# Kernel tuning notes

Hardware: AMD Instinct MI355X
Metric: run time of the kernel (lower is better)

Reference implementation:

```python
import jax, jax.numpy as jnp
import numpy as np

T, B, OBS, H, A = 256, 128, 512, 1024, 18


def setup_inputs() -> dict:
    key = jax.random.key(0)
    ks = jax.random.split(key, 9)
    s = 0.02
    return {
        "state": jax.random.normal(ks[0], (T, B, OBS), dtype=jnp.float32),
        "mask": jax.random.randint(ks[1], (T, B), 0, 2, dtype=jnp.int32),
        "W_enc": jax.random.normal(ks[2], (H, OBS), dtype=jnp.float32) * s,
        "b_enc": jnp.zeros((H,), dtype=jnp.float32),
        "W_ih": jax.random.normal(ks[3], (4 * H, H), dtype=jnp.float32) * s,
        "W_hh": jax.random.normal(ks[4], (4 * H, H), dtype=jnp.float32) * s,
        "b_ih": jnp.zeros((4 * H,), dtype=jnp.float32),
        "b_hh": jnp.zeros((4 * H,), dtype=jnp.float32),
        "W_dec": jax.random.normal(ks[5], (A, H), dtype=jnp.float32) * s,
        "b_dec": jnp.zeros((A,), dtype=jnp.float32),
    }


def reference(state, mask, W_enc, b_enc, W_ih, W_hh, b_ih, b_hh, W_dec, b_dec):
    maskf = mask.astype(state.dtype)  # (T, B)
    hidden = W_hh.shape[1]
    # encode all timesteps in one GEMM: (T,B,OBS) @ (OBS,H)
    encoded = jax.nn.relu(jnp.einsum('tbo,ho->tbh', state, W_enc) + b_enc)
    # precompute input contribution to all gates (T,B,4H)
    x_gates = jnp.einsum('tbh,gh->tbg', encoded, W_ih) + b_ih + b_hh
    h0 = jnp.zeros((state.shape[1], hidden), dtype=state.dtype)
    c0 = jnp.zeros_like(h0)

    def step(carry, inp):
        h, c = carry
        xg, m = inp  # xg: (B,4H), m: (B,)
        gates = xg + h @ W_hh.T
        i, f, g, o = jnp.split(gates, 4, axis=-1)  # PyTorch LSTMCell gate order
        i = jax.nn.sigmoid(i)
        f = jax.nn.sigmoid(f)
        g = jnp.tanh(g)
        o = jax.nn.sigmoid(o)
        c_new = (f * c + i * g) * m[:, None]
        h_new = (o * jnp.tanh(f * c + i * g)) * m[:, None]
        return (h_new, c_new), h_new

    (h, c), latent = jax.lax.scan(step, (h0, c0), (x_gates, maskf))
    # decode all timesteps in one GEMM, then apply mask
    values = jnp.einsum('tbh,ah->tba', latent, W_dec) + b_dec
    values = values * maskf[:, :, None]
    return values, h, c
```

## Files before the change

### kernel.cpp

```cpp
#include <hip/hip_runtime.h>

#define T_STEPS 256
#define BATCH   128
#define OBSD    512
#define HID     1024
#define GH      4096
#define ACTD    18
#define TBROWS  (T_STEPS*BATCH)
#define SNWG    512
#define JG      16

typedef __bf16 bf16x8_t __attribute__((ext_vector_type(8)));
typedef float  f32x4_t  __attribute__((ext_vector_type(4)));

__device__ __forceinline__ ushort f2bf(float f) {
  unsigned u = __builtin_bit_cast(unsigned, f);
  u += 0x7fffu + ((u >> 16) & 1u);
  return (ushort)(u >> 16);
}
__device__ __forceinline__ float bf2f(ushort s) {
  return __builtin_bit_cast(float, ((unsigned)s) << 16);
}
__device__ __forceinline__ f32x4_t mfma16(bf16x8_t a, bf16x8_t b, f32x4_t c) {
  return __builtin_amdgcn_mfma_f32_16x16x32_bf16(a, b, c, 0, 0, 0);
}
__device__ __forceinline__ void gl_lds16(const void* g, void* l) {
  __builtin_amdgcn_global_load_lds(
      (__attribute__((address_space(1))) void*)(g),
      (__attribute__((address_space(3))) void*)(l), 16, 0, 0);
}
__device__ __forceinline__ float sigm(float x) { return 1.f / (1.f + __expf(-x)); }
__device__ __forceinline__ float tanhf_fast(float x) {
  float e = __expf(2.f * x);
  return (e - 1.f) / (e + 1.f);
}
#define WAITVM(N) __builtin_amdgcn_s_waitcnt(0x0F70 | ((N) & 15))
__device__ __forceinline__ void wait_vm0() { __builtin_amdgcn_s_waitcnt(0x0F70); }

__global__ void cast_bf16_kernel(const float* __restrict__ in, ushort* __restrict__ out, int n4) {
  int i = blockIdx.x * blockDim.x + threadIdx.x;
  int stride = gridDim.x * blockDim.x;
  for (; i < n4; i += stride) {
    float4 v = reinterpret_cast<const float4*>(in)[i];
    ushort4 o;
    o.x = f2bf(v.x); o.y = f2bf(v.y); o.z = f2bf(v.z); o.w = f2bf(v.w);
    reinterpret_cast<ushort4*>(out)[i] = o;
  }
}

__global__ void cast_permute_wih_kernel(const float* __restrict__ in, ushort* __restrict__ out) {
  int idx = blockIdx.x * 256 + threadIdx.x;
  int rowd = idx >> 7;
  int c8 = (idx & 127) << 3;
  int g = rowd & 3, hid = rowd >> 2;
  const float* src = in + ((size_t)g * HID + hid) * HID + c8;
  ushort* dst = out + (size_t)rowd * HID + c8;
#pragma unroll
  for (int i = 0; i < 8; ++i) dst[i] = f2bf(src[i]);
}

__global__ void bias_perm_kernel(const float* __restrict__ bih, const float* __restrict__ bhh,
                                 float* __restrict__ out) {
  int i = blockIdx.x * 256 + threadIdx.x;
  int g = i & 3, hid = i >> 2;
  out[i] = bih[g * HID + hid] + bhh[g * HID + hid];
}

__global__ __launch_bounds__(256) void gemm_bt_kernel(
    const ushort* __restrict__ A, const ushort* __restrict__ Bt,
    const float* __restrict__ bias1,
    ushort* __restrict__ C, int M, int N, int K, int relu,
    const int* __restrict__ omask, float* __restrict__ ovals)
{
  __shared__ ushort la[128 * 64];
  __shared__ ushort lb[128 * 64];

  const int tid  = threadIdx.x;
  const int lane = tid & 63;
  const int w    = tid >> 6;
  const int wm   = w >> 1, wn = w & 1;
  const int nwg = gridDim.x;
  const int q8  = nwg >> 3;
  const int bid = (blockIdx.x & 7) * q8 + (blockIdx.x >> 3);
  const int ntiles = N >> 7;
  const int bm = bid / ntiles, bn = bid % ntiles;
  const size_t m0 = (size_t)bm << 7, n0 = (size_t)bn << 7;

  const int lrow = lane & 15;
  const int lk   = (lane >> 4) << 3;
  const int wavebase = (tid & ~63);

  f32x4_t acc[4][4];
  const f32x4_t zero = {0.f, 0.f, 0.f, 0.f};
#pragma unroll
  for (int i = 0; i < 4; ++i)
#pragma unroll
    for (int j = 0; j < 4; ++j) acc[i][j] = zero;

  for (int k0 = 0; k0 < K; k0 += 64) {
#pragma unroll
    for (int p = 0; p < 4; ++p) {
      int c = p * 256 + tid;
      int r = c >> 3;
      int q = (c & 7) << 3;
      gl_lds16(A + (m0 + r) * (size_t)K + k0 + q, la + (size_t)(p * 256 + wavebase) * 8);
      gl_lds16(Bt + (n0 + r) * (size_t)K + k0 + q, lb + (size_t)(p * 256 + wavebase) * 8);
    }
    __syncthreads();
#pragma unroll
    for (int kk = 0; kk < 64; kk += 32) {
      bf16x8_t af[4], bfr[4];
#pragma unroll
      for (int i = 0; i < 4; ++i)
        af[i] = *(const bf16x8_t*)(la + (wm * 64 + i * 16 + lrow) * 64 + kk + lk);
#pragma unroll
      for (int j = 0; j < 4; ++j)
        bfr[j] = *(const bf16x8_t*)(lb + (wn * 64 + j * 16 + lrow) * 64 + kk + lk);
#pragma unroll
      for (int i = 0; i < 4; ++i)
#pragma unroll
        for (int j = 0; j < 4; ++j)
          acc[i][j] = mfma16(af[i], bfr[j], acc[i][j]);
    }
    __syncthreads();
  }

  const int crow0 = (lane >> 4) * 4;
  if (ovals) {
#pragma unroll
    for (int j = 0; j < 4; ++j) {
      int col = wn * 64 + j * 16 + lrow;
      if (col < ACTD) {
        float bv = bias1[col];
#pragma unroll
        for (int i = 0; i < 4; ++i) {
#pragma unroll
          for (int r = 0; r < 4; ++r) {
            size_t row = m0 + wm * 64 + i * 16 + crow0 + r;
            float mv = (float)omask[row];
            ovals[row * ACTD + col] = (acc[i][j][r] + bv) * mv;
          }
        }
      }
    }
    return;
  }
#pragma unroll
  for (int j = 0; j < 4; ++j) {
    int col = (int)n0 + wn * 64 + j * 16 + lrow;
    float bv = bias1 ? bias1[col] : 0.f;
#pragma unroll
    for (int i = 0; i < 4; ++i) {
#pragma unroll
      for (int r = 0; r < 4; ++r) {
        size_t row = m0 + wm * 64 + i * 16 + crow0 + r;
        float v = acc[i][j][r] + bv;
        if (relu) v = fmaxf(v, 0.f);
        C[row * (size_t)N + col] = f2bf(v);
      }
    }
  }
}

__global__ __launch_bounds__(512, 2) void gemm256_kernel(
    const ushort* __restrict__ A, const ushort* __restrict__ Bt,
    const float* __restrict__ bias,
    ushort* __restrict__ C, int M, int N, int K, int relu)
{
  __shared__ __align__(16) ushort lds[2][2][16384];

  const int tid  = threadIdx.x;
  const int lane = tid & 63;
  const int wid  = tid >> 6;
  const int wm   = wid >> 2, wn = wid & 3;
  const int nwg  = gridDim.x;
  const int q8   = nwg >> 3;
  const int bid  = (blockIdx.x & 7) * q8 + (blockIdx.x >> 3);
  const int ntiles = N >> 8;
  const int bm = bid / ntiles, bn = bid % ntiles;
  const size_t m0 = (size_t)bm << 8, n0 = (size_t)bn << 8;

  const int lrow = lane & 15;
  const int lkg  = lane >> 4;

  int srow[4], sgsr[4];
#pragma unroll
  for (int q = 0; q < 4; ++q) {
    int s = (q * 8 + wid) * 64 + lane;
    srow[q] = s >> 3;
    sgsr[q] = (s & 7) ^ ((s >> 3) & 7);
  }

#define STAGE256(BUF, KT) do {                                                \
    const size_t kb_ = (size_t)(KT) * 64;                                     \
    _Pragma("unroll")                                                         \
    for (int q = 0; q < 4; ++q) {                                             \
      gl_lds16(A  + (m0 + srow[q]) * (size_t)K + kb_ + sgsr[q] * 8,           \
               &lds[BUF][0][(q * 8 + wid) * 512]);                            \
      gl_lds16(Bt + (n0 + srow[q]) * (size_t)K + kb_ + sgsr[q] * 8,           \
               &lds[BUF][1][(q * 8 + wid) * 512]);                            \
    }                                                                         \
  } while (0)

  f32x4_t acc[8][4];
  const f32x4_t zero = {0.f, 0.f, 0.f, 0.f};
#pragma unroll
  for (int f = 0; f < 8; ++f)
#pragma unroll
    for (int n = 0; n < 4; ++n) acc[f][n] = zero;

  const int nkt = K >> 6;
  STAGE256(0, 0);
  STAGE256(1, 1);

  for (int kt = 0; kt < nkt; ++kt) {
    const int buf = kt & 1;
    if (kt + 1 < nkt) WAITVM(8); else WAITVM(0);
    __builtin_amdgcn_s_barrier();
    __builtin_amdgcn_sched_barrier(0);
#pragma unroll
    for (int p = 0; p < 4; ++p) {
      const int kk = p >> 1, mg = p & 1;
      bf16x8_t av[4], bv[4];
#pragma unroll
      for (int f = 0; f < 4; ++f) {
        int ar = wm * 128 + (mg * 4 + f) * 16 + lrow;
        int ags = (kk * 4 + lkg) ^ (ar & 7);
        av[f] = *(const bf16x8_t*)&lds[buf][0][ar * 64 + ags * 8];
      }
#pragma unroll
      for (int n = 0; n < 4; ++n) {
        int br = wn * 64 + n * 16 + lrow;
        int bgs = (kk * 4 + lkg) ^ (br & 7);
        bv[n] = *(const bf16x8_t*)&lds[buf][1][br * 64 + bgs * 8];
      }
      __builtin_amdgcn_s_setprio(1);
#pragma unroll
      for (int f = 0; f < 4; ++f)
#pragma unroll
        for (int n = 0; n < 4; ++n)
          acc[mg * 4 + f][n] = mfma16(av[f], bv[n], acc[mg * 4 + f][n]);
      __builtin_amdgcn_s_setprio(0);
    }
    __builtin_amdgcn_s_barrier();
    if (kt + 2 < nkt) STAGE256(buf, kt + 2);
  }
#undef STAGE256

  const int crow0 = lkg * 4;
#pragma unroll
  for (int n = 0; n < 4; ++n) {
    int col = (int)n0 + wn * 64 + n * 16 + lrow;
    float bvv = bias ? bias[col] : 0.f;
#pragma unroll
    for (int f = 0; f < 8; ++f) {
#pragma unroll
      for (int r = 0; r < 4; ++r) {
        size_t row = m0 + (size_t)wm * 128 + f * 16 + crow0 + r;
        float v = acc[f][n][r] + bvv;
        if (relu) v = fmaxf(v, 0.f);
        C[row * (size_t)N + col] = f2bf(v);
      }
    }
  }
}

__global__ __launch_bounds__(256, 2) void lstm_scan_kernel(
    const ushort* __restrict__ xg,
    const ushort* __restrict__ whh,
    const int* __restrict__ mask,
    const ushort* __restrict__ hinit,
    ushort* __restrict__ hseq,
    float* __restrict__ cbuf,
    float* __restrict__ outh, float* __restrict__ outc,
    unsigned* __restrict__ flags,
    int t0, int nsteps)
{
  __shared__ __align__(16) ushort pool[16 * 1024];
  __shared__ __align__(16) ushort hexch[16 * 16];

  const int tid  = threadIdx.x;
  const int lane = tid & 63;
  const int w    = tid >> 6;
  const int wg   = blockIdx.x;
  const int eg   = wg >> 6;
  const int jg   = wg & 63;
  const int j0   = jg * JG;
  const int b0   = eg * 16;

  const int lrow = lane & 15;
  const int lkg  = lane >> 4;

  bf16x8_t af[8][4];
#pragma unroll 1
  for (int p = 0; p < 4; ++p) {
    for (int c = tid; c < 16 * 128; c += 256) {
      int rl = c >> 7, gn = c & 127;
      int rr = p * 16 + rl;
      int jj = rr >> 2, g = rr & 3;
      const ushort* src = whh + ((size_t)g * HID + j0 + jj) * HID + gn * 8;
      int gnd = (gn & ~7) | ((gn & 7) ^ (rl & 7));
      *reinterpret_cast<uint4*>(&pool[rl * 1024 + gnd * 8]) =
          *reinterpret_cast<const uint4*>(src);
    }
    __syncthreads();
    if (w == p) {
#pragma unroll
      for (int kc = 0; kc < 8; ++kc)
#pragma unroll
        for (int ks = 0; ks < 4; ++ks) {
          int gA = kc * 16 + ks * 4 + lkg;
          int gAs = (gA & ~7) | ((gA & 7) ^ (lrow & 7));
          af[kc][ks] = *(const bf16x8_t*)(pool + (size_t)lrow * 1024 + gAs * 8);
        }
    }
    __syncthreads();
  }

  const int jjc = w * 4 + lkg;
  const int bl0 = lrow;

  float creg;
  if (t0 == 0) creg = 0.f;
  else creg = cbuf[(size_t)(b0 + bl0) * HID + j0 + jjc];

  const int sb = w * 4 + (lane >> 4);
  const int sq = lane & 15;
  const int gg = (sq & 8) | ((sq & 7) ^ (sb & 7));

  unsigned* myflag = flags + (size_t)(eg * 64 + jg) * 16;
  const unsigned* fpoll = flags + (size_t)(eg * 64 + lane) * 16;

  ushort4 xv;
  float mv;
  {
    xv = *(const ushort4*)(xg + (size_t)(b0 + bl0) * GH + (j0 + jjc) * 4);
    mv = (float)mask[b0 + bl0];
  }
  __builtin_amdgcn_sched_barrier(0);

#define CHUNK(KC) do {                                                         \
    WAITVM(7 - (KC));                                                          \
    __builtin_amdgcn_s_barrier();                                              \
    __builtin_amdgcn_sched_barrier(0);                                         \
    const ushort* sbuf = pool + (size_t)(KC) * 2048;                           \
    _Pragma("unroll")                                                          \
    for (int ks = 0; ks < 4; ++ks) {                                           \
      int q16 = ks * 4 + lkg;                                                  \
      int qs = (q16 & 8) | ((q16 & 7) ^ (bl0 & 7));                            \
      bf16x8_t bv = *(const bf16x8_t*)(sbuf + (size_t)bl0 * 128 + qs * 8);     \
      acc = mfma16(af[KC][ks], bv, acc);                                       \
    }                                                                          \
    __builtin_amdgcn_sched_barrier(0);                                         \
  } while (0)

  for (int tl = 0; tl < nsteps; ++tl) {
    const int gs = t0 + tl;
    const ushort* hsrc = (gs == 0)
        ? (hinit + (size_t)b0 * HID)
        : (hseq + (size_t)(gs - 1) * (BATCH * HID) + (size_t)b0 * HID);

    wait_vm0();
    __builtin_amdgcn_sched_barrier(0);

    f32x4_t acc = {0.f, 0.f, 0.f, 0.f};

#pragma unroll
    for (int kc = 0; kc < 8; ++kc)
      gl_lds16(hsrc + (size_t)sb * HID + (kc * 16 + gg) * 8,
               pool + (size_t)kc * 2048 + (size_t)w * 512);
    __builtin_amdgcn_sched_barrier(0);

    CHUNK(0); CHUNK(1); CHUNK(2); CHUNK(3);
    CHUNK(4); CHUNK(5); CHUNK(6); CHUNK(7);

    {
      float ig = sigm(acc[0] + bf2f(xv.x));
      float fg = sigm(acc[1] + bf2f(xv.y));
      float gt = tanhf_fast(acc[2] + bf2f(xv.z));
      float og = sigm(acc[3] + bf2f(xv.w));
      float cp = fg * creg + ig * gt;
      creg = cp * mv;
      float h = og * tanhf_fast(cp) * mv;
      hexch[bl0 * 16 + jjc] = f2bf(h);
      if (gs == T_STEPS - 1) {
        outh[(size_t)(b0 + bl0) * HID + j0 + jjc] = h;
        outc[(size_t)(b0 + bl0) * HID + j0 + jjc] = creg;
      }
    }
    __syncthreads();

    if (tid < 64) {
      int bl = tid >> 2, seg = tid & 3;
      unsigned long long v = *(const unsigned long long*)(&hexch[bl * 16 + seg * 4]);
      unsigned long long* dst = (unsigned long long*)(hseq +
          (size_t)gs * (BATCH * HID) + (size_t)(b0 + bl) * HID + j0 + seg * 4);
      __hip_atomic_store(dst, v, __ATOMIC_RELAXED, __HIP_MEMORY_SCOPE_AGENT);
    }

    if (tl != nsteps - 1) {
      __syncthreads();
      const unsigned tgt = (unsigned)(gs + 1);
      if (tid == 0)
        __hip_atomic_store(myflag, tgt, __ATOMIC_RELAXED, __HIP_MEMORY_SCOPE_AGENT);
      {
        const ushort* xp = xg + (size_t)(tl + 1) * BATCH * GH;
        xv = *(const ushort4*)(xp + (size_t)(b0 + bl0) * GH + (j0 + jjc) * 4);
        mv = (float)mask[(tl + 1) * BATCH + b0 + bl0];
      }
      __builtin_amdgcn_sched_barrier(0);
      if (tid < 64) {
        for (;;) {
          unsigned v = __hip_atomic_load(fpoll, __ATOMIC_RELAXED, __HIP_MEMORY_SCOPE_AGENT);
          if (__all(v >= tgt)) break;
        }
      }
      __syncthreads();
    }
  }
#undef CHUNK

  cbuf[(size_t)(b0 + bl0) * HID + j0 + jjc] = creg;
}

extern "C" void kernel_launch(void* const* d_in, const int* in_sizes, int n_in,
                              void* d_out, int out_size, void* d_ws, size_t ws_size,
                              hipStream_t stream) {
  (void)in_sizes; (void)n_in; (void)out_size;
  const float* state = (const float*)d_in[0];
  const int*   mask  = (const int*)d_in[1];
  const float* Wenc  = (const float*)d_in[2];
  const float* benc  = (const float*)d_in[3];
  const float* Wih   = (const float*)d_in[4];
  const float* Whh   = (const float*)d_in[5];
  const float* bih   = (const float*)d_in[6];
  const float* bhh   = (const float*)d_in[7];
  const float* Wdec  = (const float*)d_in[8];
  const float* bdec  = (const float*)d_in[9];

  float* out_values = (float*)d_out;
  float* out_h = out_values + (size_t)TBROWS * ACTD;
  float* out_c = out_h + (size_t)BATCH * HID;

  auto pad256 = [](size_t b) { return (b + 255) & ~(size_t)255; };

  const size_t sz_wenc  = (size_t)HID * OBSD * 2;
  const size_t sz_wih   = (size_t)GH * HID * 2;
  const size_t sz_whh   = (size_t)GH * HID * 2;
  const size_t sz_wdec  = (size_t)128 * HID * 2;
  const size_t sz_bdec  = 512;
  const size_t sz_bperm = (size_t)GH * sizeof(float);
  const size_t sz_flags = (size_t)SNWG * 16 * sizeof(unsigned);
  const size_t sz_hseq  = (size_t)TBROWS * HID * 2;
  const size_t sz_hinit = (size_t)BATCH * HID * 2;
  const size_t sz_cbuf  = (size_t)BATCH * HID * 4;
  const size_t fixed = pad256(sz_wenc) + pad256(sz_wih) + pad256(sz_whh) +
                       pad256(sz_wdec) + pad256(sz_bdec) + pad256(sz_bperm) +
                       pad256(sz_flags) + pad256(sz_hseq) + pad256(sz_hinit) +
                       pad256(sz_cbuf);

  int Tc = 8;
  {
    const int cands[6] = {256, 128, 64, 32, 16, 8};
    for (int ci = 0; ci < 6; ++ci) {
      int tc = cands[ci];
      size_t per = pad256((size_t)tc * BATCH * HID * 2)
                 + pad256((size_t)tc * BATCH * GH * 2);
      if (fixed + per <= ws_size) { Tc = tc; break; }
    }
  }
  const int nchunks = T_STEPS / Tc;
  const int crows = Tc * BATCH;

  char* ws = (char*)d_ws;
  size_t off = 0;
  auto alloc = [&](size_t b) { char* r = ws + off; off += pad256(b); return r; };
  ushort* wenc_bf  = (ushort*)alloc(sz_wenc);
  ushort* wih_perm = (ushort*)alloc(sz_wih);
  ushort* whh_bf   = (ushort*)alloc(sz_whh);
  ushort* wdec_pad = (ushort*)alloc(sz_wdec);
  float*  bdec_pad = (float*)alloc(sz_bdec);
  float*  bperm    = (float*)alloc(sz_bperm);
  unsigned* flags  = (unsigned*)alloc(sz_flags);
  ushort* hseq     = (ushort*)alloc(sz_hseq);
  ushort* hinit    = (ushort*)alloc(sz_hinit);
  float*  cbuf     = (float*)alloc(sz_cbuf);
  ushort* enc_c    = (ushort*)alloc((size_t)crows * HID * 2);
  ushort* xg_c     = (ushort*)alloc((size_t)crows * GH * 2);
  ushort* state_c  = xg_c;

  hipMemsetAsync(hinit, 0, sz_hinit, stream);
  hipMemsetAsync(flags, 0, sz_flags, stream);
  hipMemsetAsync(wdec_pad, 0, sz_wdec, stream);
  hipMemsetAsync(bdec_pad, 0, sz_bdec, stream);
  hipMemcpyAsync(bdec_pad, bdec, ACTD * sizeof(float), hipMemcpyDeviceToDevice, stream);

  auto cast = [&](const float* src, ushort* dst, size_t n) {
    int n4 = (int)(n / 4);
    int blocks = (n4 + 255) / 256;
    if (blocks > 4096) blocks = 4096;
    cast_bf16_kernel<<<blocks, 256, 0, stream>>>(src, dst, n4);
  };
  cast(Wenc, wenc_bf, (size_t)HID * OBSD);
  cast(Whh, whh_bf, (size_t)GH * HID);
  cast(Wdec, wdec_pad, (size_t)ACTD * HID);
  cast_permute_wih_kernel<<<(GH * 128) / 256, 256, 0, stream>>>(Wih, wih_perm);
  bias_perm_kernel<<<GH / 256, 256, 0, stream>>>(bih, bhh, bperm);

  for (int c = 0; c < nchunks; ++c) {
    const int t0 = c * Tc;
    cast(state + (size_t)t0 * BATCH * OBSD, state_c, (size_t)crows * OBSD);
    gemm256_kernel<<<(crows / 256) * (HID / 256), 512, 0, stream>>>(
        state_c, wenc_bf, benc, enc_c, crows, HID, OBSD, 1);
    gemm256_kernel<<<(crows / 256) * (GH / 256), 512, 0, stream>>>(
        enc_c, wih_perm, bperm, xg_c, crows, GH, HID, 0);
    lstm_scan_kernel<<<SNWG, 256, 0, stream>>>(
        xg_c, whh_bf, mask + (size_t)t0 * BATCH, hinit, hseq, cbuf,
        out_h, out_c, flags, t0, Tc);
  }

  gemm_bt_kernel<<<TBROWS / 128, 256, 0, stream>>>(
      hseq, wdec_pad, bdec_pad, nullptr, TBROWS, 128, HID, 0,
      mask, out_values);
}
```

Before: 1.297 ms.

## Split LSTM scan across 1024 two-wave workgroups and alias encoder buffer into hseq

The persistent LSTM scan now uses 1024 workgroups of 128 threads, each owning 8 hidden units instead of 16. This doubles the number of CUs taking part in the recurrent matvec and halves the W_hh slice held in registers per workgroup. Each workgroup loads twice as many h fragments per wave and polls twice as many flags, so cross-workgroup synchronisation traffic goes up. The encoder output buffer is also aliased onto the not-yet-written hseq region, freeing workspace so a larger time chunk can fit.

```diff
diff --git a/kernel.cpp b/kernel.cpp
--- a/kernel.cpp
+++ b/kernel.cpp
@@ -7,8 +7,8 @@
 #define GH      4096
 #define ACTD    18
 #define TBROWS  (T_STEPS*BATCH)
-#define SNWG    512
-#define JG      16
+#define SNWG    1024
+#define JG      8
 
 typedef __bf16 bf16x8_t __attribute__((ext_vector_type(8)));
 typedef float  f32x4_t  __attribute__((ext_vector_type(4)));
@@ -265,7 +265,7 @@
   }
 }
 
-__global__ __launch_bounds__(256, 2) void lstm_scan_kernel(
+__global__ __launch_bounds__(128, 2) void lstm_scan_kernel(
     const ushort* __restrict__ xg,
     const ushort* __restrict__ whh,
     const int* __restrict__ mask,
@@ -277,14 +277,14 @@
     int t0, int nsteps)
 {
   __shared__ __align__(16) ushort pool[16 * 1024];
-  __shared__ __align__(16) ushort hexch[16 * 16];
+  __shared__ __align__(16) ushort hexch[16 * 8];
 
   const int tid  = threadIdx.x;
   const int lane = tid & 63;
   const int w    = tid >> 6;
   const int wg   = blockIdx.x;
-  const int eg   = wg >> 6;
-  const int jg   = wg & 63;
+  const int eg   = wg >> 7;
+  const int jg   = wg & 127;
   const int j0   = jg * JG;
   const int b0   = eg * 16;
 
@@ -293,8 +293,8 @@
 
   bf16x8_t af[8][4];
 #pragma unroll 1
-  for (int p = 0; p < 4; ++p) {
-    for (int c = tid; c < 16 * 128; c += 256) {
+  for (int p = 0; p < 2; ++p) {
+    for (int c = tid; c < 16 * 128; c += 128) {
       int rl = c >> 7, gn = c & 127;
       int rr = p * 16 + rl;
       int jj = rr >> 2, g = rr & 3;
@@ -324,12 +324,18 @@
   if (t0 == 0) creg = 0.f;
   else creg = cbuf[(size_t)(b0 + bl0) * HID + j0 + jjc];
 
-  const int sb = w * 4 + (lane >> 4);
-  const int sq = lane & 15;
-  const int gg = (sq & 8) | ((sq & 7) ^ (sb & 7));
-
-  unsigned* myflag = flags + (size_t)(eg * 64 + jg) * 16;
-  const unsigned* fpoll = flags + (size_t)(eg * 64 + lane) * 16;
+  int sbq[2], ggq[2];
+#pragma unroll
+  for (int q = 0; q < 2; ++q) {
+    int s = q * 128 + w * 64 + lane;
+    int sb = s >> 4, sq = s & 15;
+    sbq[q] = sb;
+    ggq[q] = (sq & 8) | ((sq & 7) ^ (sb & 7));
+  }
+
+  unsigned* myflag = flags + (size_t)(eg * 128 + jg) * 16;
+  const unsigned* fp0 = flags + (size_t)(eg * 128 + lane) * 16;
+  const unsigned* fp1 = flags + (size_t)(eg * 128 + 64 + lane) * 16;
 
   ushort4 xv;
   float mv;
@@ -340,7 +346,7 @@
   __builtin_amdgcn_sched_barrier(0);
 
 #define CHUNK(KC) do {                                                         \
-    WAITVM(7 - (KC));                                                          \
+    WAITVM(14 - 2 * (KC));                                                     \
     __builtin_amdgcn_s_barrier();                                              \
     __builtin_amdgcn_sched_barrier(0);                                         \
     const ushort* sbuf = pool + (size_t)(KC) * 2048;                           \
@@ -366,9 +372,12 @@
     f32x4_t acc = {0.f, 0.f, 0.f, 0.f};
 
 #pragma unroll
-    for (int kc = 0; kc < 8; ++kc)
-      gl_lds16(hsrc + (size_t)sb * HID + (kc * 16 + gg) * 8,
-               pool + (size_t)kc * 2048 + (size_t)w * 512);
+    for (int kc = 0; kc < 8; ++kc) {
+      gl_lds16(hsrc + (size_t)sbq[0] * HID + (kc * 16 + ggq[0]) * 8,
+               pool + (size_t)kc * 2048 + (size_t)(w * 64) * 8);
+      gl_lds16(hsrc + (size_t)sbq[1] * HID + (kc * 16 + ggq[1]) * 8,
+               pool + (size_t)kc * 2048 + (size_t)(128 + w * 64) * 8);
+    }
     __builtin_amdgcn_sched_barrier(0);
 
     CHUNK(0); CHUNK(1); CHUNK(2); CHUNK(3);
@@ -382,7 +391,7 @@
       float cp = fg * creg + ig * gt;
       creg = cp * mv;
       float h = og * tanhf_fast(cp) * mv;
-      hexch[bl0 * 16 + jjc] = f2bf(h);
+      hexch[bl0 * 8 + jjc] = f2bf(h);
       if (gs == T_STEPS - 1) {
         outh[(size_t)(b0 + bl0) * HID + j0 + jjc] = h;
         outc[(size_t)(b0 + bl0) * HID + j0 + jjc] = creg;
@@ -390,9 +399,9 @@
     }
     __syncthreads();
 
-    if (tid < 64) {
-      int bl = tid >> 2, seg = tid & 3;
-      unsigned long long v = *(const unsigned long long*)(&hexch[bl * 16 + seg * 4]);
+    if (tid < 32) {
+      int bl = tid >> 1, seg = tid & 1;
+      unsigned long long v = *(const unsigned long long*)(&hexch[bl * 8 + seg * 4]);
       unsigned long long* dst = (unsigned long long*)(hseq +
           (size_t)gs * (BATCH * HID) + (size_t)(b0 + bl) * HID + j0 + seg * 4);
       __hip_atomic_store(dst, v, __ATOMIC_RELAXED, __HIP_MEMORY_SCOPE_AGENT);
@@ -411,8 +420,9 @@
       __builtin_amdgcn_sched_barrier(0);
       if (tid < 64) {
         for (;;) {
-          unsigned v = __hip_atomic_load(fpoll, __ATOMIC_RELAXED, __HIP_MEMORY_SCOPE_AGENT);
-          if (__all(v >= tgt)) break;
+          unsigned v0 = __hip_atomic_load(fp0, __ATOMIC_RELAXED, __HIP_MEMORY_SCOPE_AGENT);
+          unsigned v1 = __hip_atomic_load(fp1, __ATOMIC_RELAXED, __HIP_MEMORY_SCOPE_AGENT);
+          if (__all(v0 >= tgt && v1 >= tgt)) break;
         }
       }
       __syncthreads();
@@ -464,8 +474,7 @@
     const int cands[6] = {256, 128, 64, 32, 16, 8};
     for (int ci = 0; ci < 6; ++ci) {
       int tc = cands[ci];
-      size_t per = pad256((size_t)tc * BATCH * HID * 2)
-                 + pad256((size_t)tc * BATCH * GH * 2);
+      size_t per = pad256((size_t)tc * BATCH * GH * 2);
       if (fixed + per <= ws_size) { Tc = tc; break; }
     }
   }
@@ -485,7 +494,6 @@
   ushort* hseq     = (ushort*)alloc(sz_hseq);
   ushort* hinit    = (ushort*)alloc(sz_hinit);
   float*  cbuf     = (float*)alloc(sz_cbuf);
-  ushort* enc_c    = (ushort*)alloc((size_t)crows * HID * 2);
   ushort* xg_c     = (ushort*)alloc((size_t)crows * GH * 2);
   ushort* state_c  = xg_c;
 
@@ -509,12 +517,13 @@
 
   for (int c = 0; c < nchunks; ++c) {
     const int t0 = c * Tc;
+    ushort* enc_c = hseq + (size_t)t0 * BATCH * HID;
     cast(state + (size_t)t0 * BATCH * OBSD, state_c, (size_t)crows * OBSD);
     gemm256_kernel<<<(crows / 256) * (HID / 256), 512, 0, stream>>>(
         state_c, wenc_bf, benc, enc_c, crows, HID, OBSD, 1);
     gemm256_kernel<<<(crows / 256) * (GH / 256), 512, 0, stream>>>(
         enc_c, wih_perm, bperm, xg_c, crows, GH, HID, 0);
-    lstm_scan_kernel<<<SNWG, 256, 0, stream>>>(
+    lstm_scan_kernel<<<SNWG, 128, 0, stream>>>(
         xg_c, whh_bf, mask + (size_t)t0 * BATCH, hinit, hseq, cbuf,
         out_h, out_c, flags, t0, Tc);
   }
```

Result: slower. 2.050 ms (+58.1%).
